# Kernel optimization log

Measured on AMD Instinct MI355X. Metric: run time of the kernel, lower is better.

Reference implementation:

```python
import jax, jax.numpy as jnp
import numpy as np
from jax import lax

# Model dims (from init_kwargs / mamba_ssm defaults)
D_MODEL = 256
EXPAND = 2
D_INNER = EXPAND * D_MODEL      # 512
D_STATE = 64                     # ssm_rank
DT_RANK = D_MODEL // 16          # 16 (mamba_ssm default ceil(d_model/16))
D_CONV = 4
IMG = 384
PATCH = 16
BATCH = 16
NUM_CLASSES = 10
NBLK = 6                         # sum(depths) = 2+2+2
GRID = IMG // PATCH
NTOK = GRID * GRID + 1           # 577 (patches + cls token)


def setup_inputs() -> dict:
    key = jax.random.key(0)
    ks = iter(jax.random.split(key, 32))
    rn = lambda shape, s=0.02: jax.random.normal(next(ks), shape, jnp.float32) * s
    inp = {}
    inp["x"] = jax.random.normal(next(ks), (BATCH, 3, IMG, IMG), jnp.float32)
    # patch embed conv
    inp["patch_w"] = rn((D_MODEL, 3, PATCH, PATCH), 0.05)
    inp["patch_b"] = jnp.zeros((D_MODEL,), jnp.float32)
    inp["cls_token"] = rn((1, 1, D_MODEL))
    inp["pos_embed"] = rn((1, NTOK, D_MODEL))
    # stacked per-block Mamba params
    inp["norm_w"] = jnp.ones((NBLK, D_MODEL), jnp.float32)
    inp["norm_b"] = jnp.zeros((NBLK, D_MODEL), jnp.float32)
    inp["in_proj_w"] = rn((NBLK, 2 * D_INNER, D_MODEL))
    inp["conv_w"] = rn((NBLK, D_INNER, 1, D_CONV), 0.1)
    inp["conv_b"] = jnp.zeros((NBLK, D_INNER), jnp.float32)
    inp["x_proj_w"] = rn((NBLK, DT_RANK + 2 * D_STATE, D_INNER))
    inp["dt_proj_w"] = rn((NBLK, D_INNER, DT_RANK), 0.1)
    inp["dt_proj_b"] = rn((NBLK, D_INNER), 0.5)
    # S4D-real init: A = -[1..d_state]
    inp["A_log"] = jnp.log(jnp.broadcast_to(
        jnp.arange(1, D_STATE + 1, dtype=jnp.float32), (NBLK, D_INNER, D_STATE)))
    inp["D_ssm"] = jnp.ones((NBLK, D_INNER), jnp.float32)
    inp["out_proj_w"] = rn((NBLK, D_MODEL, D_INNER))
    inp["fnorm_w"] = jnp.ones((D_MODEL,), jnp.float32)
    inp["fnorm_b"] = jnp.zeros((D_MODEL,), jnp.float32)
    inp["head_w"] = rn((NUM_CLASSES, D_MODEL))
    inp["head_b"] = jnp.zeros((NUM_CLASSES,), jnp.float32)
    return inp


def layer_norm(x, w, b, eps=1e-5):
    mu = jnp.mean(x, axis=-1, keepdims=True)
    var = jnp.mean(jnp.square(x - mu), axis=-1, keepdims=True)
    return (x - mu) * lax.rsqrt(var + eps) * w + b


def causal_dwconv(x, w, b):
    # x: (B, di, L), w: (di, 1, K) depthwise; causal left pad K-1
    K = w.shape[-1]
    y = lax.conv_general_dilated(x, w, (1,), [(K - 1, 0)],
                                 dimension_numbers=("NCH", "OIH", "NCH"),
                                 feature_group_count=x.shape[1])
    return y + b[None, :, None]


def selective_scan(u, dt, A, Bm, Cm, Dp):
    # u, dt: (B, L, di); Bm, Cm: (B, L, ds); A: (di, ds); Dp: (di,)
    def step(h, inp):
        dt_t, B_t, C_t, u_t = inp                       # (B,di),(B,ds),(B,ds),(B,di)
        dA = jnp.exp(dt_t[:, :, None] * A)              # (B, di, ds)
        h = dA * h + (dt_t * u_t)[:, :, None] * B_t[:, None, :]
        y = jnp.einsum('bds,bs->bd', h, C_t)
        return h, y
    h0 = jnp.zeros((u.shape[0], A.shape[0], A.shape[1]), u.dtype)
    _, ys = lax.scan(step, h0, (dt.transpose(1, 0, 2), Bm.transpose(1, 0, 2),
                                Cm.transpose(1, 0, 2), u.transpose(1, 0, 2)))
    return ys.transpose(1, 0, 2) + u * Dp


def mamba_block(x, nw, nb, inw, cw, cb, xpw, dtw, dtb, alog, dp, ow):
    res = x
    x = layer_norm(x, nw, nb)
    xz = jnp.einsum('bld,ed->ble', x, inw)              # (B, L, 2*di)
    xi, z = jnp.split(xz, 2, axis=-1)
    xi = causal_dwconv(xi.transpose(0, 2, 1), cw, cb).transpose(0, 2, 1)
    xi = jax.nn.silu(xi)
    dbl = jnp.einsum('bld,ed->ble', xi, xpw)            # (B, L, dt_rank + 2*ds)
    dtr = dbl[..., :DT_RANK]
    Bm = dbl[..., DT_RANK:DT_RANK + D_STATE]
    Cm = dbl[..., DT_RANK + D_STATE:]
    dt = jax.nn.softplus(jnp.einsum('blr,dr->bld', dtr, dtw) + dtb)
    A = -jnp.exp(alog)
    y = selective_scan(xi, dt, A, Bm, Cm, dp)
    y = y * jax.nn.silu(z)
    return res + jnp.einsum('bld,ed->ble', y, ow)


def reference(x, patch_w, patch_b, cls_token, pos_embed,
              norm_w, norm_b, in_proj_w, conv_w, conv_b, x_proj_w,
              dt_proj_w, dt_proj_b, A_log, D_ssm, out_proj_w,
              fnorm_w, fnorm_b, head_w, head_b):
    B = x.shape[0]
    h = lax.conv_general_dilated(x, patch_w, (PATCH, PATCH), 'VALID',
                                 dimension_numbers=("NCHW", "OIHW", "NCHW"))
    h = h + patch_b[None, :, None, None]
    h = h.reshape(B, D_MODEL, -1).transpose(0, 2, 1)    # (B, G*G, D)
    h = jnp.concatenate([jnp.broadcast_to(cls_token, (B, 1, D_MODEL)), h], axis=1)
    h = h + pos_embed
    for i in range(NBLK):
        h = mamba_block(h, norm_w[i], norm_b[i], in_proj_w[i], conv_w[i], conv_b[i],
                        x_proj_w[i], dt_proj_w[i], dt_proj_b[i], A_log[i], D_ssm[i],
                        out_proj_w[i])
    h = layer_norm(h, fnorm_w, fnorm_b)
    return h[:, 0] @ head_w.T + head_b
```

## Files before the change

### kernel.cpp

```cpp
#include <hip/hip_runtime.h>
#include <hip/hip_bf16.h>
#include <cstdint>
#include <cstddef>

#define L_TOK 577
#define DM 256
#define DI 512
#define DS_ 64
#define NROWS (16*577)
#define PROWS (16*576)
#define NCH 37

typedef float f32x4v __attribute__((ext_vector_type(4)));
typedef __bf16 bf16x8 __attribute__((ext_vector_type(8)));
typedef __bf16 bf16x4 __attribute__((ext_vector_type(4)));

__device__ __forceinline__ float fast_exp2(float x) {
#if __has_builtin(__builtin_amdgcn_exp2f)
    return __builtin_amdgcn_exp2f(x);
#else
    return __expf(x * 0.6931471805599453f);
#endif
}

__device__ __forceinline__ bf16x4 to_bf4(float a, float b, float c, float d) {
    bf16x4 r; r[0]=(__bf16)a; r[1]=(__bf16)b; r[2]=(__bf16)c; r[3]=(__bf16)d; return r;
}

__global__ __launch_bounds__(256)
void k_cvt(const float* __restrict__ s, __bf16* __restrict__ d, int n4)
{
    for (int i = blockIdx.x*256 + threadIdx.x; i < n4; i += gridDim.x*256) {
        float4 v = *reinterpret_cast<const float4*>(s + (size_t)i*4);
        *reinterpret_cast<bf16x4*>(d + (size_t)i*4) = to_bf4(v.x, v.y, v.z, v.w);
    }
}

__global__ __launch_bounds__(256)
void k_gemm(const __bf16* __restrict__ A, int lda,
            const __bf16* __restrict__ B, int ldb,
            void* __restrict__ Cvp, int ldc,
            int M, int N, int K, int cmode)
{
    __shared__ char sA[128*128];
    __shared__ char sB[128*128];
    const int tid  = threadIdx.x;
    const int lane = tid & 63;
    const int wave = tid >> 6;
    const int wr = wave >> 1, wc = wave & 1;
    const int tm = blockIdx.y * 128, tn = blockIdx.x * 128;

    f32x4v acc[4][4];
#pragma unroll
    for (int m = 0; m < 4; ++m)
#pragma unroll
        for (int n = 0; n < 4; ++n) acc[m][n] = (f32x4v){0.f, 0.f, 0.f, 0.f};

    const int nk = K >> 6;
    for (int kt = 0; kt < nk; ++kt) {
        const int k0 = kt << 6;
        __syncthreads();
#pragma unroll
        for (int i = 0; i < 4; ++i) {
            int c = tid + (i << 8);
            int row = c >> 3, slot = c & 7;
            int gr = tm + row; gr = gr < M ? gr : M - 1;
            bf16x8 va = *reinterpret_cast<const bf16x8*>(A + (size_t)gr*lda + k0 + (slot<<3));
            *reinterpret_cast<bf16x8*>(&sA[(row << 7) + ((slot ^ (row & 7)) << 4)]) = va;
        }
#pragma unroll
        for (int i = 0; i < 4; ++i) {
            int c = tid + (i << 8);
            int row = c >> 3, slot = c & 7;
            int gr = tn + row; gr = gr < N ? gr : N - 1;
            bf16x8 vb = *reinterpret_cast<const bf16x8*>(B + (size_t)gr*ldb + k0 + (slot<<3));
            *reinterpret_cast<bf16x8*>(&sB[(row << 7) + ((slot ^ (row & 7)) << 4)]) = vb;
        }
        __syncthreads();

        bf16x8 af[4][2], bfr[4][2];
#pragma unroll
        for (int kk = 0; kk < 2; ++kk) {
            int sl = (kk << 2) + (lane >> 4);
#pragma unroll
            for (int m = 0; m < 4; ++m) {
                int row = (wr << 6) + (m << 4) + (lane & 15);
                af[m][kk] = *reinterpret_cast<const bf16x8*>(&sA[(row << 7) + ((sl ^ (row & 7)) << 4)]);
            }
#pragma unroll
            for (int n = 0; n < 4; ++n) {
                int row = (wc << 6) + (n << 4) + (lane & 15);
                bfr[n][kk] = *reinterpret_cast<const bf16x8*>(&sB[(row << 7) + ((sl ^ (row & 7)) << 4)]);
            }
        }
#pragma unroll
        for (int kk = 0; kk < 2; ++kk)
#pragma unroll
            for (int m = 0; m < 4; ++m)
#pragma unroll
                for (int n = 0; n < 4; ++n)
                    acc[m][n] = __builtin_amdgcn_mfma_f32_16x16x32_bf16(af[m][kk], bfr[n][kk], acc[m][n], 0, 0, 0);
    }

    float* Cf = (float*)Cvp;
    __bf16* Ch = (__bf16*)Cvp;
#pragma unroll
    for (int m = 0; m < 4; ++m) {
        int grow0 = tm + (wr << 6) + (m << 4) + ((lane >> 4) << 2);
#pragma unroll
        for (int n = 0; n < 4; ++n) {
            int gcol = tn + (wc << 6) + (n << 4) + (lane & 15);
            if (gcol < N) {
#pragma unroll
                for (int j = 0; j < 4; ++j) {
                    int grow = grow0 + j;
                    if (grow < M) {
                        size_t o = (size_t)grow * ldc + gcol;
                        float v = acc[m][n][j];
                        if (cmode == 1)      Cf[o] = v + Cf[o];
                        else if (cmode == 2) Ch[o] = (__bf16)v;
                        else                 Cf[o] = v;
                    }
                }
            }
        }
    }
}

__global__ __launch_bounds__(256)
void k_im2col(const float* __restrict__ x, __bf16* __restrict__ xcol)
{
    int id = blockIdx.x * 256 + threadIdx.x;
    int kh = id & 15;
    int ci = (id >> 4) % 3;
    int row = id / 48;
    int b = row / 576, p = row % 576;
    int py = p / 24, px = p % 24;
    const float* src = x + ((size_t)(b*3 + ci)*384 + py*16 + kh)*384 + px*16;
    __bf16* dst = xcol + (size_t)row*768 + ci*256 + kh*16;
#pragma unroll
    for (int j = 0; j < 4; ++j) {
        float4 v = *reinterpret_cast<const float4*>(src + j*4);
        *reinterpret_cast<bf16x4*>(dst + j*4) = to_bf4(v.x, v.y, v.z, v.w);
    }
}

__global__ __launch_bounds__(256)
void k_assemble(const float* __restrict__ Ctmp, const float* __restrict__ pb,
                const float* __restrict__ cls, const float* __restrict__ pos,
                float* __restrict__ h_tok)
{
    int i4 = blockIdx.x * 256 + threadIdx.x;
    int c4 = i4 & 63;
    int tok = (i4 >> 6) % 577;
    int b = i4 / (577*64);
    float4 pv = *reinterpret_cast<const float4*>(pos + tok*256 + c4*4);
    float4 r;
    if (tok == 0) {
        float4 cv = *reinterpret_cast<const float4*>(cls + c4*4);
        r.x = cv.x + pv.x; r.y = cv.y + pv.y; r.z = cv.z + pv.z; r.w = cv.w + pv.w;
    } else {
        float4 t = *reinterpret_cast<const float4*>(Ctmp + (size_t)(b*576 + tok - 1)*256 + c4*4);
        float4 bb = *reinterpret_cast<const float4*>(pb + c4*4);
        r.x = t.x + bb.x + pv.x; r.y = t.y + bb.y + pv.y;
        r.z = t.z + bb.z + pv.z; r.w = t.w + bb.w + pv.w;
    }
    *reinterpret_cast<float4*>(h_tok + (size_t)i4*4) = r;
}

__global__ __launch_bounds__(256)
void k_ln(const float* __restrict__ X, const float* __restrict__ w,
          const float* __restrict__ bb, __bf16* __restrict__ O)
{
    int lane = threadIdx.x & 63;
    int row = blockIdx.x * 4 + (threadIdx.x >> 6);
    const float4 v = *reinterpret_cast<const float4*>(X + (size_t)row*256 + lane*4);
    float s1 = v.x + v.y + v.z + v.w;
    float s2 = v.x*v.x + v.y*v.y + v.z*v.z + v.w*v.w;
#pragma unroll
    for (int o2 = 32; o2; o2 >>= 1) { s1 += __shfl_xor(s1, o2); s2 += __shfl_xor(s2, o2); }
    float mu = s1 * (1.f/256.f);
    float var = s2 * (1.f/256.f) - mu*mu;
    float rs = rsqrtf(var + 1e-5f);
    float4 wv = *reinterpret_cast<const float4*>(w + lane*4);
    float4 bv = *reinterpret_cast<const float4*>(bb + lane*4);
    *reinterpret_cast<bf16x4*>(O + (size_t)row*256 + lane*4) =
        to_bf4((v.x - mu)*rs*wv.x + bv.x, (v.y - mu)*rs*wv.y + bv.y,
               (v.z - mu)*rs*wv.z + bv.z, (v.w - mu)*rs*wv.w + bv.w);
}

__global__ __launch_bounds__(256)
void k_conv(const __bf16* __restrict__ xz, const float* __restrict__ cw,
            const float* __restrict__ cb, __bf16* __restrict__ xi)
{
    int gw = blockIdx.x * 4 + (threadIdx.x >> 6);
    int lane = threadIdx.x & 63;
    int tc = gw % 73;
    int eg = (gw / 73) & 7;
    int b  = gw / (73*8);
    int e = eg*64 + lane;
    float4 wv = *reinterpret_cast<const float4*>(cw + e*4);
    float bias = cb[e];
    int t0 = tc * 8;
    float xv[11];
#pragma unroll
    for (int j = 0; j < 11; ++j) {
        int t = t0 - 3 + j;
        xv[j] = (t >= 0 && t < 577) ? (float)xz[(size_t)(b*577 + t)*1024 + e] : 0.f;
    }
#pragma unroll
    for (int j = 0; j < 8; ++j) {
        int t = t0 + j;
        if (t < 577) {
            float a = wv.x*xv[j] + wv.y*xv[j+1] + wv.z*xv[j+2] + wv.w*xv[j+3] + bias;
            float sgm = 1.f / (1.f + __expf(-a));
            xi[(size_t)(b*577 + t)*512 + e] = (__bf16)(a * sgm);
        }
    }
}

__global__ __launch_bounds__(256)
void k_dtfuse(const float* __restrict__ dbl, const float* __restrict__ dtw,
              const float* __restrict__ dtb, const __bf16* __restrict__ xi,
              float* __restrict__ tri2)
{
    __shared__ float dtr[16][16];
    const int tid = threadIdx.x;
    const int b    = blockIdx.x / 74;
    const int rr   = blockIdx.x % 74;
    const int tc   = rr >> 1;
    const int e    = ((rr & 1) << 8) + tid;
    const int nj   = (tc == 36) ? 1 : 16;
    {
        int j = tid >> 4, r = tid & 15;
        if (j < nj)
            dtr[j][r] = dbl[((size_t)(b*577) + tc*16 + j)*144 + r];
    }
    __syncthreads();
    const float* wp = dtw + e*16;
    float4 w0 = *reinterpret_cast<const float4*>(wp);
    float4 w1 = *reinterpret_cast<const float4*>(wp + 4);
    float4 w2 = *reinterpret_cast<const float4*>(wp + 8);
    float4 w3 = *reinterpret_cast<const float4*>(wp + 12);
    float bias = dtb[e];
    float* outp = tri2 + ((size_t)(b*37 + tc)*512 + e)*32;
    for (int j = 0; j < nj; ++j) {
        const float* dr = dtr[j];
        float accv = bias;
        accv += w0.x*dr[0] + w0.y*dr[1] + w0.z*dr[2] + w0.w*dr[3];
        accv += w1.x*dr[4] + w1.y*dr[5] + w1.z*dr[6] + w1.w*dr[7];
        accv += w2.x*dr[8] + w2.y*dr[9] + w2.z*dr[10] + w2.w*dr[11];
        accv += w3.x*dr[12] + w3.y*dr[13] + w3.z*dr[14] + w3.w*dr[15];
        float sp = accv > 20.f ? accv : log1pf(__expf(accv));
        float u = (float)xi[((size_t)(b*577) + tc*16 + j)*512 + e];
        float2 o; o.x = sp; o.y = sp * u;
        *reinterpret_cast<float2*>(outp + j*2) = o;
    }
}

__global__ __launch_bounds__(256, 4)
void k_scan(const float* __restrict__ tri2, const float* __restrict__ dbl,
            const float* __restrict__ A_log, float* __restrict__ ych)
{
    __shared__ float tp[4*16*65];
    const int tid  = threadIdx.x;
    const int lane = tid & 63;
    const int wv   = tid >> 6;
    const int bb   = blockIdx.x >> 6;
    const int d0   = __builtin_amdgcn_readfirstlane(((blockIdx.x & 63) << 3) + (wv << 1));
    const float al0 = -__expf(A_log[(size_t)d0*64 + lane]) * 1.44269504f;
    const float al1 = -__expf(A_log[(size_t)(d0+1)*64 + lane]) * 1.44269504f;
    const float2* trp = reinterpret_cast<const float2*>(tri2)
                      + ((size_t)bb*NCH*512 + d0)*16;
    const float* Bb = dbl + (size_t)bb*577*144 + 16 + lane;
    float* yo = ych + ((size_t)bb*NCH*512 + d0)*16;
    float* tpw = tp + wv*(16*65);
    const int g = lane >> 4, tt = lane & 15;
    float h0 = 0.f, h1 = 0.f;

    for (int c = 0; c < 36; ++c) {
        const int t0 = c << 4;
        float p0[16], p1[16];
#pragma unroll
        for (int j = 0; j < 16; ++j) {
            float2 u0 = trp[(size_t)c*8192 + j];
            float2 u1 = trp[(size_t)c*8192 + 16 + j];
            float Bv = Bb[(size_t)(t0 + j)*144];
            float Cv = Bb[(size_t)(t0 + j)*144 + 64];
            h0 = __builtin_fmaf(fast_exp2(u0.x*al0), h0, u0.y*Bv);
            h1 = __builtin_fmaf(fast_exp2(u1.x*al1), h1, u1.y*Bv);
            p0[j] = h0 * Cv;
            p1[j] = h1 * Cv;
        }
#pragma unroll
        for (int j = 0; j < 16; ++j) tpw[j*65 + lane] = p0[j];
        float s0 = 0.f;
        {
            const float* rp = tpw + tt*65 + g*16;
#pragma unroll
            for (int k = 0; k < 16; ++k) s0 += rp[k];
        }
        s0 += __shfl_xor(s0, 16); s0 += __shfl_xor(s0, 32);
        if (lane < 16) yo[(size_t)c*8192 + tt] = s0;
#pragma unroll
        for (int j = 0; j < 16; ++j) tpw[j*65 + lane] = p1[j];
        float s1 = 0.f;
        {
            const float* rp = tpw + tt*65 + g*16;
#pragma unroll
            for (int k = 0; k < 16; ++k) s1 += rp[k];
        }
        s1 += __shfl_xor(s1, 16); s1 += __shfl_xor(s1, 32);
        if (lane < 16) yo[(size_t)c*8192 + 16 + tt] = s1;
    }
    {
        float2 u0 = trp[(size_t)36*8192];
        float2 u1 = trp[(size_t)36*8192 + 16];
        float Bv = Bb[(size_t)576*144];
        float Cv = Bb[(size_t)576*144 + 64];
        h0 = __builtin_fmaf(fast_exp2(u0.x*al0), h0, u0.y*Bv);
        h1 = __builtin_fmaf(fast_exp2(u1.x*al1), h1, u1.y*Bv);
        float q0 = h0 * Cv, q1 = h1 * Cv;
#pragma unroll
        for (int o2 = 32; o2; o2 >>= 1) { q0 += __shfl_xor(q0, o2); q1 += __shfl_xor(q1, o2); }
        if (lane == 0) {
            yo[(size_t)36*8192] = q0;
            yo[(size_t)36*8192 + 16] = q1;
        }
    }
}

__global__ __launch_bounds__(256)
void k_gate(const float* __restrict__ ych, const __bf16* __restrict__ xz,
            const __bf16* __restrict__ xi, const float* __restrict__ Dp,
            __bf16* __restrict__ yb)
{
    int i4 = blockIdx.x * 256 + threadIdx.x;
    int row = i4 >> 7;
    int c4 = i4 & 127;
    int b = row / 577, t = row % 577;
    int cc = t >> 4, tt = t & 15;
    int d = c4 << 2;
    const float* yp = ych + ((size_t)(b*NCH + cc)*512 + d)*16 + tt;
    float y0 = yp[0], y1 = yp[16], y2 = yp[32], y3 = yp[48];
    bf16x4 u4 = *reinterpret_cast<const bf16x4*>(xi + (size_t)row*512 + d);
    bf16x4 z4 = *reinterpret_cast<const bf16x4*>(xz + (size_t)row*1024 + 512 + d);
    float4 dv = *reinterpret_cast<const float4*>(Dp + d);
    float z0 = (float)z4[0], z1 = (float)z4[1], z2 = (float)z4[2], z3 = (float)z4[3];
    float g0 = z0 / (1.f + __expf(-z0)), g1 = z1 / (1.f + __expf(-z1));
    float g2 = z2 / (1.f + __expf(-z2)), g3 = z3 / (1.f + __expf(-z3));
    *reinterpret_cast<bf16x4*>(yb + (size_t)row*512 + d) =
        to_bf4((y0 + (float)u4[0]*dv.x) * g0, (y1 + (float)u4[1]*dv.y) * g1,
               (y2 + (float)u4[2]*dv.z) * g2, (y3 + (float)u4[3]*dv.w) * g3);
}

__global__ __launch_bounds__(256)
void k_head(const float* __restrict__ h_tok, const float* __restrict__ fw,
            const float* __restrict__ fb, const float* __restrict__ hw,
            const float* __restrict__ hb, float* __restrict__ out)
{
    int b = blockIdx.x, tid = threadIdx.x;
    __shared__ float sv[256];
    __shared__ float sr[16];
    float v = h_tok[(size_t)b*577*256 + tid];
    float s1 = v, s2 = v*v;
#pragma unroll
    for (int o2 = 32; o2; o2 >>= 1) { s1 += __shfl_xor(s1, o2); s2 += __shfl_xor(s2, o2); }
    int wave = tid >> 6;
    if ((tid & 63) == 0) { sr[wave] = s1; sr[wave + 8] = s2; }
    __syncthreads();
    float t1 = sr[0] + sr[1] + sr[2] + sr[3];
    float t2 = sr[8] + sr[9] + sr[10] + sr[11];
    float mu = t1 * (1.f/256.f);
    float var = t2 * (1.f/256.f) - mu*mu;
    float rs = rsqrtf(var + 1e-5f);
    sv[tid] = (v - mu)*rs*fw[tid] + fb[tid];
    __syncthreads();
    if (tid < 10) {
        float acc = hb[tid];
        for (int d2 = 0; d2 < 256; ++d2) acc += sv[d2]*hw[tid*256 + d2];
        out[b*10 + tid] = acc;
    }
}

extern "C" void kernel_launch(void* const* d_in, const int* in_sizes, int n_in,
                              void* d_out, int out_size, void* d_ws, size_t ws_size,
                              hipStream_t stream)
{
    const float* x         = (const float*)d_in[0];
    const float* patch_w   = (const float*)d_in[1];
    const float* patch_b   = (const float*)d_in[2];
    const float* cls_tok   = (const float*)d_in[3];
    const float* pos_emb   = (const float*)d_in[4];
    const float* norm_w    = (const float*)d_in[5];
    const float* norm_b    = (const float*)d_in[6];
    const float* in_proj_w = (const float*)d_in[7];
    const float* conv_w    = (const float*)d_in[8];
    const float* conv_b    = (const float*)d_in[9];
    const float* x_proj_w  = (const float*)d_in[10];
    const float* dt_proj_w = (const float*)d_in[11];
    const float* dt_proj_b = (const float*)d_in[12];
    const float* A_log     = (const float*)d_in[13];
    const float* D_ssm     = (const float*)d_in[14];
    const float* out_proj_w= (const float*)d_in[15];
    const float* fnorm_w   = (const float*)d_in[16];
    const float* fnorm_b   = (const float*)d_in[17];
    const float* head_w    = (const float*)d_in[18];
    const float* head_b    = (const float*)d_in[19];
    float* out = (float*)d_out;

    char* ws = (char*)d_ws;
    size_t off = 0;
    auto carveB = [&](size_t bytes) -> char* {
        char* p = ws + off;
        off += (bytes + 255) & ~(size_t)255;
        return p;
    };
    float*  h_tok = (float*) carveB((size_t)NROWS*DM*4);
    __bf16* xln   = (__bf16*)carveB((size_t)NROWS*DM*2);
    __bf16* xz    = (__bf16*)carveB((size_t)NROWS*1024*2);
    __bf16* xi    = (__bf16*)carveB((size_t)NROWS*DI*2);
    float*  dbl   = (float*) carveB((size_t)NROWS*144*4);
    float*  tri2  = (float*) carveB((size_t)16*NCH*DI*32*4);
    float*  ych   = (float*) carveB((size_t)16*NCH*DI*16*4);
    __bf16* yb    = (__bf16*)carveB((size_t)NROWS*DI*2);
    __bf16* pwb   = (__bf16*)carveB((size_t)196608*2);
    __bf16* iwb   = (__bf16*)carveB((size_t)6*1024*DM*2);
    __bf16* xwb   = (__bf16*)carveB((size_t)6*144*DI*2);
    __bf16* owb   = (__bf16*)carveB((size_t)6*DM*DI*2);
    __bf16* xcol  = xz;
    float*  Ctmp  = ych;

    k_cvt<<<192, 256, 0, stream>>>(patch_w, pwb, 196608/4);
    k_cvt<<<1024, 256, 0, stream>>>(in_proj_w, iwb, (6*1024*DM)/4);
    k_cvt<<<432, 256, 0, stream>>>(x_proj_w, xwb, (6*144*DI)/4);
    k_cvt<<<768, 256, 0, stream>>>(out_proj_w, owb, (6*DM*DI)/4);

    k_im2col<<<1728, 256, 0, stream>>>(x, xcol);
    {
        dim3 g(2, 72);
        k_gemm<<<g, 256, 0, stream>>>(xcol, 768, pwb, 768, Ctmp, 256, PROWS, 256, 768, 0);
    }
    k_assemble<<<2308, 256, 0, stream>>>(Ctmp, patch_b, cls_tok, pos_emb, h_tok);

    for (int i = 0; i < 6; ++i) {
        k_ln<<<2308, 256, 0, stream>>>(h_tok, norm_w + i*DM, norm_b + i*DM, xln);
        {
            dim3 g(8, 73);
            k_gemm<<<g, 256, 0, stream>>>(xln, DM, iwb + (size_t)i*1024*DM, DM,
                                          xz, 1024, NROWS, 1024, DM, 2);
        }
        k_conv<<<2336, 256, 0, stream>>>(xz, conv_w + (size_t)i*DI*4, conv_b + i*DI, xi);
        {
            dim3 g(2, 73);
            k_gemm<<<g, 256, 0, stream>>>(xi, DI, xwb + (size_t)i*144*DI, DI,
                                          dbl, 144, NROWS, 144, DI, 0);
        }
        k_dtfuse<<<16*NCH*2, 256, 0, stream>>>(dbl, dt_proj_w + (size_t)i*DI*16, dt_proj_b + i*DI,
                                               xi, tri2);
        k_scan<<<1024, 256, 0, stream>>>(tri2, dbl, A_log + (size_t)i*DI*DS_, ych);
        k_gate<<<4616, 256, 0, stream>>>(ych, xz, xi, D_ssm + i*DI, yb);
        {
            dim3 g(2, 73);
            k_gemm<<<g, 256, 0, stream>>>(yb, DI, owb + (size_t)i*DM*DI, DI,
                                          h_tok, DM, NROWS, DM, DI, 1);
        }
    }
    k_head<<<16, 256, 0, stream>>>(h_tok, fnorm_w, fnorm_b, head_w, head_b, out);
}
```

Before: 1.694 ms.

## Add 64x64 GEMM tile, bf16 x_proj output, prefetched scan loads, fused weight cvt

Adds a 64x64-tile MFMA GEMM and uses it for the patch-embed, x_proj and out_proj GEMMs, so the narrow-N problems launch more blocks and fill more CUs. The x_proj output (dt/B/C) is now stored in bf16, which halves its traffic, and the scan and dtfuse kernels read it as bf16. The scan loop is restructured to prefetch the next chunk's B/C into registers while the current chunk is processed, and the two state reductions now use separate shared buffers. The four weight-conversion launches are merged into one. Storing B/C and dt rank in bf16 lowers precision in the scan inputs.

```diff
diff --git a/kernel.cpp b/kernel.cpp
--- a/kernel.cpp
+++ b/kernel.cpp
@@ -28,11 +28,20 @@
 }
 
 __global__ __launch_bounds__(256)
-void k_cvt(const float* __restrict__ s, __bf16* __restrict__ d, int n4)
-{
-    for (int i = blockIdx.x*256 + threadIdx.x; i < n4; i += gridDim.x*256) {
-        float4 v = *reinterpret_cast<const float4*>(s + (size_t)i*4);
-        *reinterpret_cast<bf16x4*>(d + (size_t)i*4) = to_bf4(v.x, v.y, v.z, v.w);
+void k_cvtall(const float* __restrict__ s0, __bf16* __restrict__ d0, int n0,
+              const float* __restrict__ s1, __bf16* __restrict__ d1, int n1,
+              const float* __restrict__ s2, __bf16* __restrict__ d2, int n2,
+              const float* __restrict__ s3, __bf16* __restrict__ d3, int n3)
+{
+    int total = n0 + n1 + n2 + n3;
+    for (int i = blockIdx.x*256 + threadIdx.x; i < total; i += gridDim.x*256) {
+        const float* s; __bf16* d; int k = i;
+        if (k < n0) { s = s0; d = d0; }
+        else if ((k -= n0) < n1) { s = s1; d = d1; }
+        else if ((k -= n1) < n2) { s = s2; d = d2; }
+        else { k -= n2; s = s3; d = d3; }
+        float4 v = *reinterpret_cast<const float4*>(s + (size_t)k*4);
+        *reinterpret_cast<bf16x4*>(d + (size_t)k*4) = to_bf4(v.x, v.y, v.z, v.w);
     }
 }
 
@@ -110,6 +119,97 @@
 #pragma unroll
         for (int n = 0; n < 4; ++n) {
             int gcol = tn + (wc << 6) + (n << 4) + (lane & 15);
+            if (gcol < N) {
+#pragma unroll
+                for (int j = 0; j < 4; ++j) {
+                    int grow = grow0 + j;
+                    if (grow < M) {
+                        size_t o = (size_t)grow * ldc + gcol;
+                        float v = acc[m][n][j];
+                        if (cmode == 1)      Cf[o] = v + Cf[o];
+                        else if (cmode == 2) Ch[o] = (__bf16)v;
+                        else                 Cf[o] = v;
+                    }
+                }
+            }
+        }
+    }
+}
+
+__global__ __launch_bounds__(256)
+void k_gemm64(const __bf16* __restrict__ A, int lda,
+              const __bf16* __restrict__ B, int ldb,
+              void* __restrict__ Cvp, int ldc,
+              int M, int N, int K, int cmode)
+{
+    __shared__ char sA[64*128];
+    __shared__ char sB[64*128];
+    const int tid  = threadIdx.x;
+    const int lane = tid & 63;
+    const int wave = tid >> 6;
+    const int wr = wave >> 1, wc = wave & 1;
+    const int tm = blockIdx.y * 64, tn = blockIdx.x * 64;
+
+    f32x4v acc[2][2];
+#pragma unroll
+    for (int m = 0; m < 2; ++m)
+#pragma unroll
+        for (int n = 0; n < 2; ++n) acc[m][n] = (f32x4v){0.f, 0.f, 0.f, 0.f};
+
+    const int nk = K >> 6;
+    for (int kt = 0; kt < nk; ++kt) {
+        const int k0 = kt << 6;
+        __syncthreads();
+#pragma unroll
+        for (int i = 0; i < 2; ++i) {
+            int c = tid + (i << 8);
+            int row = c >> 3, slot = c & 7;
+            int gr = tm + row; gr = gr < M ? gr : M - 1;
+            bf16x8 va = *reinterpret_cast<const bf16x8*>(A + (size_t)gr*lda + k0 + (slot<<3));
+            *reinterpret_cast<bf16x8*>(&sA[(row << 7) + ((slot ^ (row & 7)) << 4)]) = va;
+        }
+#pragma unroll
+        for (int i = 0; i < 2; ++i) {
+            int c = tid + (i << 8);
+            int row = c >> 3, slot = c & 7;
+            int gr = tn + row; gr = gr < N ? gr : N - 1;
+            bf16x8 vb = *reinterpret_cast<const bf16x8*>(B + (size_t)gr*ldb + k0 + (slot<<3));
+            *reinterpret_cast<bf16x8*>(&sB[(row << 7) + ((slot ^ (row & 7)) << 4)]) = vb;
+        }
+        __syncthreads();
+
+        bf16x8 af[2][2], bfr[2][2];
+#pragma unroll
+        for (int kk = 0; kk < 2; ++kk) {
+            int sl = (kk << 2) + (lane >> 4);
+#pragma unroll
+            for (int m = 0; m < 2; ++m) {
+                int row = (wr << 5) + (m << 4) + (lane & 15);
+                af[m][kk] = *reinterpret_cast<const bf16x8*>(&sA[(row << 7) + ((sl ^ (row & 7)) << 4)]);
+            }
+#pragma unroll
+            for (int n = 0; n < 2; ++n) {
+                int row = (wc << 5) + (n << 4) + (lane & 15);
+                bfr[n][kk] = *reinterpret_cast<const bf16x8*>(&sB[(row << 7) + ((sl ^ (row & 7)) << 4)]);
+            }
+        }
+#pragma unroll
+        for (int kk = 0; kk < 2; ++kk)
+#pragma unroll
+            for (int m = 0; m < 2; ++m)
+#pragma unroll
+                for (int n = 0; n < 2; ++n)
+                    acc[m][n] = __builtin_amdgcn_mfma_f32_16x16x32_bf16(af[m][kk], bfr[n][kk], acc[m][n], 0, 0, 0);
+    }
+
+    float* Cf = (float*)Cvp;
+    __bf16* Ch = (__bf16*)Cvp;
+#pragma unroll
+    for (int m = 0; m < 2; ++m) {
+        int grow0 = tm + (wr << 5) + (m << 4) + ((lane >> 4) << 2);
+#pragma unroll
+        for (int n = 0; n < 2; ++n) {
+            int gcol = tn + (wc << 5) + (n << 4) + (lane & 15);
             if (gcol < N) {
 #pragma unroll
                 for (int j = 0; j < 4; ++j) {
@@ -220,7 +320,7 @@
 }
 
 __global__ __launch_bounds__(256)
-void k_dtfuse(const float* __restrict__ dbl, const float* __restrict__ dtw,
+void k_dtfuse(const __bf16* __restrict__ dbl, const float* __restrict__ dtw,
               const float* __restrict__ dtb, const __bf16* __restrict__ xi,
               float* __restrict__ tri2)
 {
@@ -234,7 +334,7 @@
     {
         int j = tid >> 4, r = tid & 15;
         if (j < nj)
-            dtr[j][r] = dbl[((size_t)(b*577) + tc*16 + j)*144 + r];
+            dtr[j][r] = (float)dbl[((size_t)(b*577) + tc*16 + j)*144 + r];
     }
     __syncthreads();
     const float* wp = dtw + e*16;
@@ -258,11 +358,41 @@
     }
 }
 
+#define LOADBC(c, Ba, Ca) do { \
+    _Pragma("unroll") \
+    for (int j_ = 0; j_ < 16; ++j_) { \
+        Ba[j_] = (float)Bb[(size_t)((c)*16 + j_)*144]; \
+        Ca[j_] = (float)Bb[(size_t)((c)*16 + j_)*144 + 64]; \
+    } } while (0)
+
+#define PROCC(c, Ba, Ca) do { \
+    const float2* tc_ = trp + (size_t)(c)*8192; \
+    _Pragma("unroll") \
+    for (int j_ = 0; j_ < 16; ++j_) { \
+        float2 u0 = tc_[j_]; \
+        float2 u1 = tc_[16 + j_]; \
+        h0 = __builtin_fmaf(fast_exp2(u0.x*al0), h0, u0.y*Ba[j_]); \
+        h1 = __builtin_fmaf(fast_exp2(u1.x*al1), h1, u1.y*Ba[j_]); \
+        tpwA[j_*65 + lane] = h0 * Ca[j_]; \
+        tpwB[j_*65 + lane] = h1 * Ca[j_]; \
+    } \
+    float s0 = 0.f, s1 = 0.f; \
+    { const float* rpA = tpwA + tt*65 + g*16; \
+      const float* rpB = tpwB + tt*65 + g*16; \
+      _Pragma("unroll") \
+      for (int k_ = 0; k_ < 16; ++k_) { s0 += rpA[k_]; s1 += rpB[k_]; } } \
+    s0 += __shfl_xor(s0, 16); s0 += __shfl_xor(s0, 32); \
+    s1 += __shfl_xor(s1, 16); s1 += __shfl_xor(s1, 32); \
+    if (lane < 16) { \
+        yo[(size_t)(c)*8192 + tt] = s0; \
+        yo[(size_t)(c)*8192 + 16 + tt] = s1; \
+    } } while (0)
+
 __global__ __launch_bounds__(256, 4)
-void k_scan(const float* __restrict__ tri2, const float* __restrict__ dbl,
+void k_scan(const float* __restrict__ tri2, const __bf16* __restrict__ dbl,
             const float* __restrict__ A_log, float* __restrict__ ych)
 {
-    __shared__ float tp[4*16*65];
+    __shared__ float tp[8*16*65];
     const int tid  = threadIdx.x;
     const int lane = tid & 63;
     const int wv   = tid >> 6;
@@ -272,52 +402,27 @@
     const float al1 = -__expf(A_log[(size_t)(d0+1)*64 + lane]) * 1.44269504f;
     const float2* trp = reinterpret_cast<const float2*>(tri2)
                       + ((size_t)bb*NCH*512 + d0)*16;
-    const float* Bb = dbl + (size_t)bb*577*144 + 16 + lane;
+    const __bf16* Bb = dbl + (size_t)bb*577*144 + 16 + lane;
     float* yo = ych + ((size_t)bb*NCH*512 + d0)*16;
-    float* tpw = tp + wv*(16*65);
+    float* tpwA = tp + (wv*2)*(16*65);
+    float* tpwB = tp + (wv*2 + 1)*(16*65);
     const int g = lane >> 4, tt = lane & 15;
     float h0 = 0.f, h1 = 0.f;
-
-    for (int c = 0; c < 36; ++c) {
-        const int t0 = c << 4;
-        float p0[16], p1[16];
-#pragma unroll
-        for (int j = 0; j < 16; ++j) {
-            float2 u0 = trp[(size_t)c*8192 + j];
-            float2 u1 = trp[(size_t)c*8192 + 16 + j];
-            float Bv = Bb[(size_t)(t0 + j)*144];
-            float Cv = Bb[(size_t)(t0 + j)*144 + 64];
-            h0 = __builtin_fmaf(fast_exp2(u0.x*al0), h0, u0.y*Bv);
-            h1 = __builtin_fmaf(fast_exp2(u1.x*al1), h1, u1.y*Bv);
-            p0[j] = h0 * Cv;
-            p1[j] = h1 * Cv;
-        }
-#pragma unroll
-        for (int j = 0; j < 16; ++j) tpw[j*65 + lane] = p0[j];
-        float s0 = 0.f;
-        {
-            const float* rp = tpw + tt*65 + g*16;
-#pragma unroll
-            for (int k = 0; k < 16; ++k) s0 += rp[k];
-        }
-        s0 += __shfl_xor(s0, 16); s0 += __shfl_xor(s0, 32);
-        if (lane < 16) yo[(size_t)c*8192 + tt] = s0;
-#pragma unroll
-        for (int j = 0; j < 16; ++j) tpw[j*65 + lane] = p1[j];
-        float s1 = 0.f;
-        {
-            const float* rp = tpw + tt*65 + g*16;
-#pragma unroll
-            for (int k = 0; k < 16; ++k) s1 += rp[k];
-        }
-        s1 += __shfl_xor(s1, 16); s1 += __shfl_xor(s1, 32);
-        if (lane < 16) yo[(size_t)c*8192 + 16 + tt] = s1;
+    float B0[16], C0[16], B1[16], C1[16];
+
+    LOADBC(0, B0, C0);
+    for (int cc = 0; cc < 18; ++cc) {
+        const int c0 = cc << 1;
+        LOADBC(c0 + 1, B1, C1);
+        PROCC(c0, B0, C0);
+        if (cc < 17) LOADBC(c0 + 2, B0, C0);
+        PROCC(c0 + 1, B1, C1);
     }
     {
         float2 u0 = trp[(size_t)36*8192];
         float2 u1 = trp[(size_t)36*8192 + 16];
-        float Bv = Bb[(size_t)576*144];
-        float Cv = Bb[(size_t)576*144 + 64];
+        float Bv = (float)Bb[(size_t)576*144];
+        float Cv = (float)Bb[(size_t)576*144 + 64];
         h0 = __builtin_fmaf(fast_exp2(u0.x*al0), h0, u0.y*Bv);
         h1 = __builtin_fmaf(fast_exp2(u1.x*al1), h1, u1.y*Bv);
         float q0 = h0 * Cv, q1 = h1 * Cv;
@@ -420,7 +525,7 @@
     __bf16* xln   = (__bf16*)carveB((size_t)NROWS*DM*2);
     __bf16* xz    = (__bf16*)carveB((size_t)NROWS*1024*2);
     __bf16* xi    = (__bf16*)carveB((size_t)NROWS*DI*2);
-    float*  dbl   = (float*) carveB((size_t)NROWS*144*4);
+    __bf16* dbl   = (__bf16*)carveB((size_t)NROWS*144*2);
     float*  tri2  = (float*) carveB((size_t)16*NCH*DI*32*4);
     float*  ych   = (float*) carveB((size_t)16*NCH*DI*16*4);
     __bf16* yb    = (__bf16*)carveB((size_t)NROWS*DI*2);
@@ -431,15 +536,15 @@
     __bf16* xcol  = xz;
     float*  Ctmp  = ych;
 
-    k_cvt<<<192, 256, 0, stream>>>(patch_w, pwb, 196608/4);
-    k_cvt<<<1024, 256, 0, stream>>>(in_proj_w, iwb, (6*1024*DM)/4);
-    k_cvt<<<432, 256, 0, stream>>>(x_proj_w, xwb, (6*144*DI)/4);
-    k_cvt<<<768, 256, 0, stream>>>(out_proj_w, owb, (6*DM*DI)/4);
+    k_cvtall<<<2048, 256, 0, stream>>>(patch_w, pwb, 196608/4,
+                                       in_proj_w, iwb, (6*1024*DM)/4,
+                                       x_proj_w, xwb, (6*144*DI)/4,
+                                       out_proj_w, owb, (6*DM*DI)/4);
 
     k_im2col<<<1728, 256, 0, stream>>>(x, xcol);
     {
-        dim3 g(2, 72);
-        k_gemm<<<g, 256, 0, stream>>>(xcol, 768, pwb, 768, Ctmp, 256, PROWS, 256, 768, 0);
+        dim3 g(4, 144);
+        k_gemm64<<<g, 256, 0, stream>>>(xcol, 768, pwb, 768, Ctmp, 256, PROWS, 256, 768, 0);
     }
     k_assemble<<<2308, 256, 0, stream>>>(Ctmp, patch_b, cls_tok, pos_emb, h_tok);
 
@@ -452,18 +557,18 @@
         }
         k_conv<<<2336, 256, 0, stream>>>(xz, conv_w + (size_t)i*DI*4, conv_b + i*DI, xi);
         {
-            dim3 g(2, 73);
-            k_gemm<<<g, 256, 0, stream>>>(xi, DI, xwb + (size_t)i*144*DI, DI,
-                                          dbl, 144, NROWS, 144, DI, 0);
+            dim3 g(3, 145);
+            k_gemm64<<<g, 256, 0, stream>>>(xi, DI, xwb + (size_t)i*144*DI, DI,
+                                            dbl, 144, NROWS, 144, DI, 2);
         }
         k_dtfuse<<<16*NCH*2, 256, 0, stream>>>(dbl, dt_proj_w + (size_t)i*DI*16, dt_proj_b + i*DI,
                                                xi, tri2);
         k_scan<<<1024, 256, 0, stream>>>(tri2, dbl, A_log + (size_t)i*DI*DS_, ych);
         k_gate<<<4616, 256, 0, stream>>>(ych, xz, xi, D_ssm + i*DI, yb);
         {
-            dim3 g(2, 73);
-            k_gemm<<<g, 256, 0, stream>>>(yb, DI, owb + (size_t)i*DM*DI, DI,
-                                          h_tok, DM, NROWS, DM, DI, 1);
+            dim3 g(4, 145);
+            k_gemm64<<<g, 256, 0, stream>>>(yb, DI, owb + (size_t)i*DM*DI, DI,
+                                            h_tok, DM, NROWS, DM, DI, 1);
         }
     }
     k_head<<<16, 256, 0, stream>>>(h_tok, fnorm_w, fnorm_b, head_w, head_b, out);
```

Result: faster. 1.578 ms (-6.8%).
